# Kernel tuning notes

Measured on AMD Instinct MI355X. Metric: run time of the kernel, lower is better.

Reference implementation:

```python
import jax, jax.numpy as jnp
import numpy as np

N_BINS = 10
A_CONST = 0.4
C_CONST = 500.0


def entropy(v, n=N_BINS):
    # Faithful to the torch loop: p_i = mean(v >= lo + i*s and v < lo + (i+1)*s),
    # entropy -= p*log(p) for p != 0. Vectorized over the n bins.
    v = v.reshape(-1)
    lo = v.min()
    hi = v.max()
    scale = (hi - lo) / n
    idx = jnp.arange(n, dtype=v.dtype)
    lower = lo + idx * scale                    # [n]
    upper = lower + scale                       # [n]
    mask = (v[None, :] >= lower[:, None]) & (v[None, :] < upper[:, None])  # [n, len(v)]
    p = mask.sum(axis=1).astype(v.dtype) / v.shape[0]
    safe_p = jnp.where(p > 0, p, 1.0)
    return -jnp.sum(jnp.where(p > 0, p * jnp.log(safe_p), 0.0))


def unite(p_i, p_j, w_assess, b_assess):
    # w_local = sigmoid(Linear(|p_i - p_j|)); w_global scalar from entropy gap.
    w_local = jax.nn.sigmoid(jnp.abs(p_i - p_j) @ w_assess.T + b_assess)
    w_global = A_CONST / jnp.pi * jnp.arctan(C_CONST * (entropy(p_i) - entropy(p_j))) + 0.5
    w = w_global * w_local + (1.0 - w_global)
    return p_i * w + p_j * (1.0 - w)


def setup_inputs() -> dict:
    key = jax.random.key(0)
    ks = jax.random.split(key, 11)
    B, S, H, L = 64, 512, 1024, 3
    s = 1.0 / np.sqrt(H)
    return {
        "x": jax.random.normal(ks[0], (B, S, H), jnp.float32),
        "base_dense_w": jax.random.normal(ks[1], (H, H), jnp.float32) * s,
        "base_dense_b": jax.random.normal(ks[2], (H,), jnp.float32) * s,
        "base_out_w": jax.random.normal(ks[3], (L, H), jnp.float32) * s,
        "base_out_b": jax.random.normal(ks[4], (L,), jnp.float32) * s,
        "graft_dense_w": jax.random.normal(ks[5], (H, H), jnp.float32) * s,
        "graft_out_w": jax.random.normal(ks[6], (L, H), jnp.float32) * s,
        "dense_assess_w": jax.random.normal(ks[7], (H, H), jnp.float32) * s,
        "dense_assess_b": jax.random.normal(ks[8], (H,), jnp.float32) * s,
        "out_assess_w": jax.random.normal(ks[9], (H, H), jnp.float32) * s,
        "out_assess_b": jax.random.normal(ks[10], (H,), jnp.float32) * s,
    }


def reference(x, base_dense_w, base_dense_b, base_out_w, base_out_b,
              graft_dense_w, graft_out_w,
              dense_assess_w, dense_assess_b, out_assess_w, out_assess_b):
    # roberta branch; dropout is identity (eval mode)
    h = x[:, 0, :]  # [B, H] CLS token
    # layer 0: dense
    pu0 = unite(base_dense_w, graft_dense_w, dense_assess_w, dense_assess_b)
    h = jnp.tanh(h @ pu0.T + base_dense_b)
    # layer 1: out_proj (final -> return)
    pu1 = unite(base_out_w, graft_out_w, out_assess_w, out_assess_b)
    return h @ pu1.T + base_out_b
```

## Files before the change

kernel.cpp:

```cpp
#include <hip/hip_runtime.h>
#include <hip/hip_bf16.h>
#include <math.h>


#define NBINS 10
typedef short bf8v __attribute__((ext_vector_type(8)));
typedef float f32x4 __attribute__((ext_vector_type(4)));

#define AST(p, v) __hip_atomic_store((p), (v), __ATOMIC_RELAXED, __HIP_MEMORY_SCOPE_AGENT)
#define ALD(p)    __hip_atomic_load((p), __ATOMIC_RELAXED, __HIP_MEMORY_SCOPE_AGENT)

static __device__ __forceinline__ unsigned short f2bf(float f) {
    __hip_bfloat16 h = __float2bfloat16(f);
    return __builtin_bit_cast(unsigned short, h);
}

#define GL2LDS(gp, lp) __builtin_amdgcn_global_load_lds(                       \
    (__attribute__((address_space(1))) void*)(gp),                             \
    (__attribute__((address_space(3))) void*)(lp), 16, 0, 0)

static __device__ __forceinline__ void stage_slot(const unsigned short* __restrict__ src,
                                                  short* dst, int s, int row0, int k0) {
    int r = s >> 3, g = (s & 7) ^ (r & 7);
    GL2LDS(src + (size_t)(row0 + r) * 1024 + k0 + g * 8, dst + s * 8);
}
static __device__ __forceinline__ bf8v fr(const short* lds, int row, int G) {
    return ((const bf8v*)lds)[row * 8 + (G ^ (row & 7))];
}

static __device__ __forceinline__ float ent_bins(const unsigned* bins, float N) {
    float s = 0.0f;
    for (int b = 0; b < NBINS; b++) {
        float p = __fdiv_rn((float)ALD(&bins[b]), N);
        if (p > 0.0f) s += p * logf(p);
    }
    return -s;
}

__global__ __launch_bounds__(256) void k_prep(
    const float* __restrict__ x, const float* __restrict__ bdw, const float* __restrict__ bow,
    const float* __restrict__ gdw, const float* __restrict__ gow, const float* __restrict__ daw,
    const float* __restrict__ oaw, char* __restrict__ ws) {
    const int blk = blockIdx.x, t = threadIdx.x;
    const int lane = t & 63, wid = t >> 6;
    float* ws_f = (float*)ws;
    unsigned* ws_u = (unsigned*)ws;
    float* slots = ws_f + 576;
    float* S1    = ws_f + 1600;
    unsigned short* Db  = (unsigned short*)(ws + 4227072);
    unsigned short* Wb  = (unsigned short*)(ws + 6324224);
    unsigned short* x0b = (unsigned short*)(ws + 8421376);
    __shared__ float sp[256];
    __shared__ float s_small[16];

    if (blk < 256) {
        float lo0 = INFINITY, hi0 = -INFINITY, lo1 = INFINITY, hi1 = -INFINITY;
        int fbase = blk * 1024 + t;
#pragma unroll
        for (int q = 0; q < 4; q++) {
            int idx = fbase + q * 256;
            float4 a = ((const float4*)bdw)[idx];
            float4 b = ((const float4*)gdw)[idx];
            float4 w = ((const float4*)daw)[idx];
            lo0 = fminf(lo0, fminf(fminf(a.x, a.y), fminf(a.z, a.w)));
            hi0 = fmaxf(hi0, fmaxf(fmaxf(a.x, a.y), fmaxf(a.z, a.w)));
            lo1 = fminf(lo1, fminf(fminf(b.x, b.y), fminf(b.z, b.w)));
            hi1 = fmaxf(hi1, fmaxf(fmaxf(b.x, b.y), fmaxf(b.z, b.w)));
            ushort4 d, ww;
            d.x = f2bf(fabsf(a.x - b.x)); d.y = f2bf(fabsf(a.y - b.y));
            d.z = f2bf(fabsf(a.z - b.z)); d.w = f2bf(fabsf(a.w - b.w));
            ww.x = f2bf(w.x); ww.y = f2bf(w.y); ww.z = f2bf(w.z); ww.w = f2bf(w.w);
            ((ushort4*)Db)[idx] = d;
            ((ushort4*)Wb)[idx] = ww;
        }
        for (int off = 32; off; off >>= 1) {
            lo0 = fminf(lo0, __shfl_down(lo0, off));
            hi0 = fmaxf(hi0, __shfl_down(hi0, off));
            lo1 = fminf(lo1, __shfl_down(lo1, off));
            hi1 = fmaxf(hi1, __shfl_down(hi1, off));
        }
        if (lane == 0) { s_small[wid] = lo0; s_small[4 + wid] = hi0; s_small[8 + wid] = lo1; s_small[12 + wid] = hi1; }
        __syncthreads();
        if (t == 0) {
            slots[blk]       = fminf(fminf(s_small[0], s_small[1]), fminf(s_small[2], s_small[3]));
            slots[256 + blk] = fmaxf(fmaxf(s_small[4], s_small[5]), fmaxf(s_small[6], s_small[7]));
            slots[512 + blk] = fminf(fminf(s_small[8], s_small[9]), fminf(s_small[10], s_small[11]));
            slots[768 + blk] = fmaxf(fmaxf(s_small[12], s_small[13]), fmaxf(s_small[14], s_small[15]));
        }
    } else {
        const int blk2 = blk - 256;
        {
            int d = t >> 4, kq = t & 15;
            if (d < 12) {
                int r = d >> 2, c = blk2 * 4 + (d & 3);
                const float4* bo4 = (const float4*)(bow + r * 1024);
                const float4* go4 = (const float4*)(gow + r * 1024);
                const float4* oa4 = (const float4*)(oaw + c * 1024);
                float s = 0.f;
#pragma unroll
                for (int k4 = kq * 16; k4 < kq * 16 + 16; ++k4) {
                    float4 bv = bo4[k4], gv = go4[k4], wv = oa4[k4];
                    s += fabsf(bv.x - gv.x) * wv.x + fabsf(bv.y - gv.y) * wv.y +
                         fabsf(bv.z - gv.z) * wv.z + fabsf(bv.w - gv.w) * wv.w;
                }
                sp[t] = s;
            }
            __syncthreads();
            if (t < 12) {
                float s = 0.f;
#pragma unroll
                for (int q = 0; q < 16; q++) s += sp[t * 16 + q];
                S1[(t >> 2) * 1024 + blk2 * 4 + (t & 3)] = s;
            }
        }
        if (blk == 256 || blk == 257) {
            const float* p = (blk == 256) ? bow : gow;
            float lo = INFINITY, hi = -INFINITY;
#pragma unroll
            for (int q = 0; q < 12; q++) { float v = p[q * 256 + t]; lo = fminf(lo, v); hi = fmaxf(hi, v); }
            for (int off = 32; off; off >>= 1) { lo = fminf(lo, __shfl_down(lo, off)); hi = fmaxf(hi, __shfl_down(hi, off)); }
            __syncthreads();
            if (lane == 0) { s_small[wid] = lo; s_small[4 + wid] = hi; }
            __syncthreads();
            if (t == 0) {
                ws_f[8 + 2 * (blk - 256)] = fminf(fminf(s_small[0], s_small[1]), fminf(s_small[2], s_small[3]));
                ws_f[9 + 2 * (blk - 256)] = fmaxf(fmaxf(s_small[4], s_small[5]), fmaxf(s_small[6], s_small[7]));
            }
        }
        if (blk == 258) {
            ws_u[64 + t] = 0u;
            ws_u[320 + t] = 0u;
            if (t < 40) ws_u[16 + t] = 0u;
        }
        if (blk >= 260 && blk < 324) {
            int row = blk - 260;
            float4 v = ((const float4*)(x + (size_t)row * 524288))[t];
            ushort4 o; o.x = f2bf(v.x); o.y = f2bf(v.y); o.z = f2bf(v.z); o.w = f2bf(v.w);
            ((ushort4*)x0b)[row * 256 + t] = o;
        }
    }
}

__global__ __launch_bounds__(256) void k_main(
    const float* __restrict__ bdw, const float* __restrict__ gdw, const float* __restrict__ dab,
    const float* __restrict__ bow, const float* __restrict__ gow, const float* __restrict__ oab,
    char* __restrict__ ws) {
    const int blk = blockIdx.x, t = threadIdx.x;
    const int lane = t & 63, wid = t >> 6;
    const int lr = lane & 15, k8 = lane >> 4;
    const int wr = wid >> 1, wc = wid & 1;

    float* ws_f = (float*)ws;
    unsigned* ws_u = (unsigned*)ws;
    unsigned* bins  = ws_u + 16;
    unsigned* flags = ws_u + 64;
    float* slots = ws_f + 576;
    float* S1    = ws_f + 1600;
    float* pu1   = ws_f + 4736;
    float* part2 = ws_f + 8192;
    const unsigned short* Db  = (const unsigned short*)(ws + 4227072);
    const unsigned short* Wb  = (const unsigned short*)(ws + 6324224);
    const unsigned short* x0b = (const unsigned short*)(ws + 8421376);

    __shared__ short lds_a[2][2048];
    __shared__ short lds_b[2][4096];
    __shared__ short ldsT[32 * 72];
    __shared__ float s_small[16];
    __shared__ unsigned s_hist[NBINS];
    __shared__ float s_wg[2];

    {
        int m, b0, nb;
        if (blk < 240)      { m = 0; b0 = blk;       nb = 240; }
        else if (blk < 480) { m = 1; b0 = blk - 240; nb = 240; }
        else if (blk < 496) { m = 2; b0 = blk - 480; nb = 16; }
        else                { m = 3; b0 = blk - 496; nb = 16; }
        const float* p = (m == 0) ? bdw : (m == 1) ? gdw : (m == 2) ? bow : gow;
        int n = (m < 2) ? 1048576 : 3072;
        float lo, hi;
        if (m < 2) {
            float l = slots[m * 512 + t];
            float h = slots[m * 512 + 256 + t];
            for (int off = 32; off; off >>= 1) { l = fminf(l, __shfl_down(l, off)); h = fmaxf(h, __shfl_down(h, off)); }
            if (lane == 0) { s_small[wid] = l; s_small[4 + wid] = h; }
            __syncthreads();
            lo = fminf(fminf(s_small[0], s_small[1]), fminf(s_small[2], s_small[3]));
            hi = fmaxf(fmaxf(s_small[4], s_small[5]), fmaxf(s_small[6], s_small[7]));
        } else {
            lo = ws_f[8 + 2 * (m - 2)];
            hi = ws_f[9 + 2 * (m - 2)];
        }
        float scale = __fdiv_rn(__fsub_rn(hi, lo), 10.0f);
        float lower[NBINS], upper[NBINS];
#pragma unroll
        for (int b = 0; b < NBINS; b++) {
            lower[b] = __fadd_rn(lo, __fmul_rn((float)b, scale));
            upper[b] = __fadd_rn(lower[b], scale);
        }
        unsigned cn[NBINS] = {};
#pragma unroll 4
        for (int i = b0 * 256 + t; i < n; i += nb * 256) {
            float v = p[i];
#pragma unroll
            for (int b = 0; b < NBINS; b++)
                if (v >= lower[b] && v < upper[b]) cn[b]++;
        }
        if (t < NBINS) s_hist[t] = 0;
        __syncthreads();
#pragma unroll
        for (int b = 0; b < NBINS; b++)
            if (cn[b]) atomicAdd(&s_hist[b], cn[b]);
        __syncthreads();
        if (t < NBINS && s_hist[t])
            __hip_atomic_fetch_add(&bins[m * NBINS + t], s_hist[t], __ATOMIC_RELAXED, __HIP_MEMORY_SCOPE_AGENT);
    }
    __syncthreads();
    if (t == 0) AST(&flags[blk], 1u);

    const int c8 = blk & 7, rr = blk >> 3;
    const int bi = ((c8 >> 1) << 3) | (rr >> 3);
    const int bj = ((c8 & 1) << 3) | (rr & 7);
    f32x4 acc0 = {0.f, 0.f, 0.f, 0.f}, acc1 = {0.f, 0.f, 0.f, 0.f};
    {
        stage_slot(Db, lds_a[0], t, bi * 32, 0);
        stage_slot(Wb, lds_b[0], t, bj * 64, 0);
        stage_slot(Wb, lds_b[0], t + 256, bj * 64, 0);
        int cur = 0;
        for (int tt = 0; tt < 16; ++tt) {
            __syncthreads();
            if (tt + 1 < 16) {
                int k0 = (tt + 1) * 64;
                stage_slot(Db, lds_a[cur ^ 1], t, bi * 32, k0);
                stage_slot(Wb, lds_b[cur ^ 1], t, bj * 64, k0);
                stage_slot(Wb, lds_b[cur ^ 1], t + 256, bj * 64, k0);
            }
#pragma unroll
            for (int kk = 0; kk < 2; kk++) {
                bf8v a  = fr(lds_a[cur], wr * 16 + lr, kk * 4 + k8);
                bf8v b0 = fr(lds_b[cur], wc * 32 + lr, kk * 4 + k8);
                bf8v b1 = fr(lds_b[cur], wc * 32 + 16 + lr, kk * 4 + k8);
                acc0 = __builtin_amdgcn_mfma_f32_16x16x32_bf16(a, b0, acc0, 0, 0, 0);
                acc1 = __builtin_amdgcn_mfma_f32_16x16x32_bf16(a, b1, acc1, 0, 0, 0);
            }
            cur ^= 1;
        }
    }

    for (;;) {
        unsigned v0 = ALD(&flags[t]);
        unsigned v1 = ALD(&flags[t + 256]);
        if (__syncthreads_and((int)(v0 >= 1u && v1 >= 1u))) break;
        __builtin_amdgcn_s_sleep(1);
    }
    if (t == 0) {
        float e0 = ent_bins(&bins[0], 1048576.0f);
        float e1 = ent_bins(&bins[10], 1048576.0f);
        float e2 = ent_bins(&bins[20], 3072.0f);
        float e3 = ent_bins(&bins[30], 3072.0f);
        const float API = (float)(0.4 / M_PI);
        s_wg[0] = API * atanf(500.0f * (e0 - e1)) + 0.5f;
        s_wg[1] = API * atanf(500.0f * (e2 - e3)) + 0.5f;
    }
    __syncthreads();

    {
        float wg = s_wg[0];
#pragma unroll
        for (int j = 0; j < 2; j++) {
            f32x4 a = j ? acc1 : acc0;
#pragma unroll
            for (int r = 0; r < 4; r++) {
                int il = wr * 16 + k8 * 4 + r;
                int jl = wc * 32 + j * 16 + lr;
                int ig = bi * 32 + il, jg = bj * 64 + jl;
                float s = a[r] + dab[jg];
                float wl = 1.0f / (1.0f + expf(-s));
                float w = wg * wl + (1.0f - wg);
                float o = bdw[ig * 1024 + jg] * w + gdw[ig * 1024 + jg] * (1.0f - w);
                ldsT[il * 72 + jl] = (short)f2bf(o);
            }
        }
        __syncthreads();
        f32x4 ah0 = {0.f, 0.f, 0.f, 0.f}, ah1 = {0.f, 0.f, 0.f, 0.f};
#pragma unroll
        for (int ks = 0; ks < 2; ks++) {
            int cl = wc * 16 + lr;
            bf8v b = *(const bf8v*)&ldsT[cl * 72 + ks * 32 + k8 * 8];
            bf8v a0 = *(const bf8v*)&x0b[(wr * 32 + lr) * 1024 + bj * 64 + ks * 32 + k8 * 8];
            bf8v a1 = *(const bf8v*)&x0b[(wr * 32 + 16 + lr) * 1024 + bj * 64 + ks * 32 + k8 * 8];
            ah0 = __builtin_amdgcn_mfma_f32_16x16x32_bf16(a0, b, ah0, 0, 0, 0);
            ah1 = __builtin_amdgcn_mfma_f32_16x16x32_bf16(a1, b, ah1, 0, 0, 0);
        }
#pragma unroll
        for (int mi = 0; mi < 2; mi++) {
            f32x4 ah = mi ? ah1 : ah0;
#pragma unroll
            for (int r = 0; r < 4; r++) {
                int m = wr * 32 + mi * 16 + k8 * 4 + r;
                int cg = bi * 32 + wc * 16 + lr;
                part2[((size_t)(bj * 64 + m) << 10) + cg] = ah[r];
            }
        }
    }
    if (blk < 16 && t < 192) {
        int r = t >> 6, c = blk * 64 + (t & 63);
        float s1 = S1[r * 1024 + c];
        float wl = 1.0f / (1.0f + expf(-(s1 + oab[c])));
        float wg = s_wg[1];
        float w = wg * wl + (1.0f - wg);
        pu1[r * 1024 + c] = bow[r * 1024 + c] * w + gow[r * 1024 + c] * (1.0f - w);
    }
}

__global__ __launch_bounds__(256) void k_out(
    const float* __restrict__ bdb, const float* __restrict__ bob,
    float* __restrict__ out, const char* __restrict__ ws) {
    const int m = blockIdx.x, t = threadIdx.x;
    const int lane = t & 63, wid = t >> 6;
    const float* ws_f = (const float*)ws;
    const float* pu1   = ws_f + 4736;
    const float* part2 = ws_f + 8192;
    __shared__ float s_small[16];

    const int c0 = t * 4;
    f32x4 s = {0.f, 0.f, 0.f, 0.f};
#pragma unroll
    for (int b = 0; b < 16; b++)
        s += *(const f32x4*)(part2 + ((size_t)(b * 64 + m) << 10) + c0);
    float h0 = tanhf(s[0] + bdb[c0]);
    float h1 = tanhf(s[1] + bdb[c0 + 1]);
    float h2 = tanhf(s[2] + bdb[c0 + 2]);
    float h3 = tanhf(s[3] + bdb[c0 + 3]);
    float p0, p1, p2;
    {
        f32x4 q0 = *(const f32x4*)(pu1 + c0);
        f32x4 q1 = *(const f32x4*)(pu1 + 1024 + c0);
        f32x4 q2 = *(const f32x4*)(pu1 + 2048 + c0);
        p0 = h0 * q0[0] + h1 * q0[1] + h2 * q0[2] + h3 * q0[3];
        p1 = h0 * q1[0] + h1 * q1[1] + h2 * q1[2] + h3 * q1[3];
        p2 = h0 * q2[0] + h1 * q2[1] + h2 * q2[2] + h3 * q2[3];
    }
    for (int off = 32; off; off >>= 1) {
        p0 += __shfl_down(p0, off);
        p1 += __shfl_down(p1, off);
        p2 += __shfl_down(p2, off);
    }
    if (lane == 0) { s_small[wid] = p0; s_small[4 + wid] = p1; s_small[8 + wid] = p2; }
    __syncthreads();
    if (t == 0) {
        out[m * 3 + 0] = s_small[0] + s_small[1] + s_small[2] + s_small[3] + bob[0];
        out[m * 3 + 1] = s_small[4] + s_small[5] + s_small[6] + s_small[7] + bob[1];
        out[m * 3 + 2] = s_small[8] + s_small[9] + s_small[10] + s_small[11] + bob[2];
    }
}

extern "C" void kernel_launch(void* const* d_in, const int* in_sizes, int n_in,
                              void* d_out, int out_size, void* d_ws, size_t ws_size,
                              hipStream_t stream) {
    const float* x   = (const float*)d_in[0];
    const float* bdw = (const float*)d_in[1];
    const float* bdb = (const float*)d_in[2];
    const float* bow = (const float*)d_in[3];
    const float* bob = (const float*)d_in[4];
    const float* gdw = (const float*)d_in[5];
    const float* gow = (const float*)d_in[6];
    const float* daw = (const float*)d_in[7];
    const float* dab = (const float*)d_in[8];
    const float* oaw = (const float*)d_in[9];
    const float* oab = (const float*)d_in[10];
    float* out = (float*)d_out;
    char* ws = (char*)d_ws;

    k_prep<<<512, 256, 0, stream>>>(x, bdw, bow, gdw, gow, daw, oaw, ws);
    k_main<<<512, 256, 0, stream>>>(bdw, gdw, dab, bow, gow, oab, ws);
    k_out<<<64, 256, 0, stream>>>(bdb, bob, out, ws);
}
```

Baseline: 55.10 us.

## Fuse output kernel into main kernel via a second grid-wide flag barrier

Removes the separate k_out launch by having the first 64 blocks of k_main spin on a second set of per-block flags, then reduce the split-K partials, apply tanh and the 3-output projection in place. Partial-sum tiles are first staged through LDS and written as coalesced 64-bit atomic stores so they are visible across blocks. The workspace layout is shifted to make room for the new flags. This saves one kernel launch and its gap, at the cost of a spin wait that relies on all 512 blocks being co-resident.

```diff
diff --git a/kernel.cpp b/kernel.cpp
--- a/kernel.cpp
+++ b/kernel.cpp
@@ -6,6 +6,7 @@
 #define NBINS 10
 typedef short bf8v __attribute__((ext_vector_type(8)));
 typedef float f32x4 __attribute__((ext_vector_type(4)));
+typedef unsigned long long u64;
 
 #define AST(p, v) __hip_atomic_store((p), (v), __ATOMIC_RELAXED, __HIP_MEMORY_SCOPE_AGENT)
 #define ALD(p)    __hip_atomic_load((p), __ATOMIC_RELAXED, __HIP_MEMORY_SCOPE_AGENT)
@@ -45,11 +46,11 @@
     const int lane = t & 63, wid = t >> 6;
     float* ws_f = (float*)ws;
     unsigned* ws_u = (unsigned*)ws;
-    float* slots = ws_f + 576;
-    float* S1    = ws_f + 1600;
-    unsigned short* Db  = (unsigned short*)(ws + 4227072);
-    unsigned short* Wb  = (unsigned short*)(ws + 6324224);
-    unsigned short* x0b = (unsigned short*)(ws + 8421376);
+    float* slots = ws_f + 1088;
+    float* S1    = ws_f + 2112;
+    unsigned short* Db  = (unsigned short*)(ws + 4456448);
+    unsigned short* Wb  = (unsigned short*)(ws + 6553600);
+    unsigned short* x0b = (unsigned short*)(ws + 8650752);
     __shared__ float sp[256];
     __shared__ float s_small[16];
 
@@ -128,8 +129,8 @@
             }
         }
         if (blk == 258) {
-            ws_u[64 + t] = 0u;
-            ws_u[320 + t] = 0u;
+#pragma unroll
+            for (int q = 0; q < 4; q++) ws_u[64 + q * 256 + t] = 0u;
             if (t < 40) ws_u[16 + t] = 0u;
         }
         if (blk >= 260 && blk < 324) {
@@ -144,7 +145,8 @@
 __global__ __launch_bounds__(256) void k_main(
     const float* __restrict__ bdw, const float* __restrict__ gdw, const float* __restrict__ dab,
     const float* __restrict__ bow, const float* __restrict__ gow, const float* __restrict__ oab,
-    char* __restrict__ ws) {
+    const float* __restrict__ bdb, const float* __restrict__ bob,
+    float* __restrict__ out, char* __restrict__ ws) {
     const int blk = blockIdx.x, t = threadIdx.x;
     const int lane = t & 63, wid = t >> 6;
     const int lr = lane & 15, k8 = lane >> 4;
@@ -152,19 +154,21 @@
 
     float* ws_f = (float*)ws;
     unsigned* ws_u = (unsigned*)ws;
-    unsigned* bins  = ws_u + 16;
-    unsigned* flags = ws_u + 64;
-    float* slots = ws_f + 576;
-    float* S1    = ws_f + 1600;
-    float* pu1   = ws_f + 4736;
-    float* part2 = ws_f + 8192;
-    const unsigned short* Db  = (const unsigned short*)(ws + 4227072);
-    const unsigned short* Wb  = (const unsigned short*)(ws + 6324224);
-    const unsigned short* x0b = (const unsigned short*)(ws + 8421376);
+    unsigned* bins   = ws_u + 16;
+    unsigned* flags1 = ws_u + 64;
+    unsigned* flags2 = ws_u + 576;
+    float* slots = ws_f + 1088;
+    float* S1    = ws_f + 2112;
+    float* pu1   = ws_f + 5248;
+    float* part2 = ws_f + 16384;
+    const unsigned short* Db  = (const unsigned short*)(ws + 4456448);
+    const unsigned short* Wb  = (const unsigned short*)(ws + 6553600);
+    const unsigned short* x0b = (const unsigned short*)(ws + 8650752);
 
     __shared__ short lds_a[2][2048];
     __shared__ short lds_b[2][4096];
     __shared__ short ldsT[32 * 72];
+    __shared__ float ldsP[64 * 33];
     __shared__ float s_small[16];
     __shared__ unsigned s_hist[NBINS];
     __shared__ float s_wg[2];
@@ -215,7 +219,7 @@
             __hip_atomic_fetch_add(&bins[m * NBINS + t], s_hist[t], __ATOMIC_RELAXED, __HIP_MEMORY_SCOPE_AGENT);
     }
     __syncthreads();
-    if (t == 0) AST(&flags[blk], 1u);
+    if (t == 0) AST(&flags1[blk], 1u);
 
     const int c8 = blk & 7, rr = blk >> 3;
     const int bi = ((c8 >> 1) << 3) | (rr >> 3);
@@ -247,8 +251,8 @@
     }
 
     for (;;) {
-        unsigned v0 = ALD(&flags[t]);
-        unsigned v1 = ALD(&flags[t + 256]);
+        unsigned v0 = ALD(&flags1[t]);
+        unsigned v1 = ALD(&flags1[t + 256]);
         if (__syncthreads_and((int)(v0 >= 1u && v1 >= 1u))) break;
         __builtin_amdgcn_s_sleep(1);
     }
@@ -295,10 +299,18 @@
         for (int mi = 0; mi < 2; mi++) {
             f32x4 ah = mi ? ah1 : ah0;
 #pragma unroll
-            for (int r = 0; r < 4; r++) {
-                int m = wr * 32 + mi * 16 + k8 * 4 + r;
-                int cg = bi * 32 + wc * 16 + lr;
-                part2[((size_t)(bj * 64 + m) << 10) + cg] = ah[r];
+            for (int r = 0; r < 4; r++)
+                ldsP[(wr * 32 + mi * 16 + k8 * 4 + r) * 33 + wc * 16 + lr] = ah[r];
+        }
+        __syncthreads();
+        {
+            int m = t >> 2, c0 = (t & 3) * 8;
+            const float* row = &ldsP[m * 33 + c0];
+            float* gp = part2 + ((size_t)(bj * 64 + m) << 10) + bi * 32 + c0;
+#pragma unroll
+            for (int q = 0; q < 4; q++) {
+                u64 u = ((u64)__float_as_uint(row[2 * q + 1]) << 32) | __float_as_uint(row[2 * q]);
+                AST((u64*)(gp + 2 * q), u);
             }
         }
     }
@@ -308,49 +320,56 @@
         float wl = 1.0f / (1.0f + expf(-(s1 + oab[c])));
         float wg = s_wg[1];
         float w = wg * wl + (1.0f - wg);
-        pu1[r * 1024 + c] = bow[r * 1024 + c] * w + gow[r * 1024 + c] * (1.0f - w);
-    }
-}
-
-__global__ __launch_bounds__(256) void k_out(
-    const float* __restrict__ bdb, const float* __restrict__ bob,
-    float* __restrict__ out, const char* __restrict__ ws) {
-    const int m = blockIdx.x, t = threadIdx.x;
-    const int lane = t & 63, wid = t >> 6;
-    const float* ws_f = (const float*)ws;
-    const float* pu1   = ws_f + 4736;
-    const float* part2 = ws_f + 8192;
-    __shared__ float s_small[16];
-
-    const int c0 = t * 4;
-    f32x4 s = {0.f, 0.f, 0.f, 0.f};
-#pragma unroll
-    for (int b = 0; b < 16; b++)
-        s += *(const f32x4*)(part2 + ((size_t)(b * 64 + m) << 10) + c0);
-    float h0 = tanhf(s[0] + bdb[c0]);
-    float h1 = tanhf(s[1] + bdb[c0 + 1]);
-    float h2 = tanhf(s[2] + bdb[c0 + 2]);
-    float h3 = tanhf(s[3] + bdb[c0 + 3]);
-    float p0, p1, p2;
-    {
-        f32x4 q0 = *(const f32x4*)(pu1 + c0);
-        f32x4 q1 = *(const f32x4*)(pu1 + 1024 + c0);
-        f32x4 q2 = *(const f32x4*)(pu1 + 2048 + c0);
-        p0 = h0 * q0[0] + h1 * q0[1] + h2 * q0[2] + h3 * q0[3];
-        p1 = h0 * q1[0] + h1 * q1[1] + h2 * q1[2] + h3 * q1[3];
-        p2 = h0 * q2[0] + h1 * q2[1] + h2 * q2[2] + h3 * q2[3];
-    }
-    for (int off = 32; off; off >>= 1) {
-        p0 += __shfl_down(p0, off);
-        p1 += __shfl_down(p1, off);
-        p2 += __shfl_down(p2, off);
-    }
-    if (lane == 0) { s_small[wid] = p0; s_small[4 + wid] = p1; s_small[8 + wid] = p2; }
+        AST(&pu1[r * 1024 + c], bow[r * 1024 + c] * w + gow[r * 1024 + c] * (1.0f - w));
+    }
     __syncthreads();
-    if (t == 0) {
-        out[m * 3 + 0] = s_small[0] + s_small[1] + s_small[2] + s_small[3] + bob[0];
-        out[m * 3 + 1] = s_small[4] + s_small[5] + s_small[6] + s_small[7] + bob[1];
-        out[m * 3 + 2] = s_small[8] + s_small[9] + s_small[10] + s_small[11] + bob[2];
+    if (t == 0) AST(&flags2[blk], 1u);
+
+    if (blk < 64) {
+        for (;;) {
+            unsigned v0 = ALD(&flags2[t]);
+            unsigned v1 = ALD(&flags2[t + 256]);
+            if (__syncthreads_and((int)(v0 >= 1u && v1 >= 1u))) break;
+            __builtin_amdgcn_s_sleep(1);
+        }
+        const int m = blk, c0 = t * 4;
+        float s0 = 0, s1 = 0, s2 = 0, s3 = 0;
+#pragma unroll
+        for (int b = 0; b < 16; b++) {
+            const float* pp = part2 + ((size_t)(b * 64 + m) << 10) + c0;
+            u64 u0 = ALD((const u64*)pp);
+            u64 u1 = ALD((const u64*)(pp + 2));
+            s0 += __uint_as_float((unsigned)u0); s1 += __uint_as_float((unsigned)(u0 >> 32));
+            s2 += __uint_as_float((unsigned)u1); s3 += __uint_as_float((unsigned)(u1 >> 32));
+        }
+        float h0 = tanhf(s0 + bdb[c0]);
+        float h1 = tanhf(s1 + bdb[c0 + 1]);
+        float h2 = tanhf(s2 + bdb[c0 + 2]);
+        float h3 = tanhf(s3 + bdb[c0 + 3]);
+        float p0, p1, p2;
+        {
+            u64 a0 = ALD((const u64*)(pu1 + c0)),        a1 = ALD((const u64*)(pu1 + c0 + 2));
+            u64 b0 = ALD((const u64*)(pu1 + 1024 + c0)), b1 = ALD((const u64*)(pu1 + 1024 + c0 + 2));
+            u64 d0 = ALD((const u64*)(pu1 + 2048 + c0)), d1 = ALD((const u64*)(pu1 + 2048 + c0 + 2));
+            p0 = h0 * __uint_as_float((unsigned)a0) + h1 * __uint_as_float((unsigned)(a0 >> 32)) +
+                 h2 * __uint_as_float((unsigned)a1) + h3 * __uint_as_float((unsigned)(a1 >> 32));
+            p1 = h0 * __uint_as_float((unsigned)b0) + h1 * __uint_as_float((unsigned)(b0 >> 32)) +
+                 h2 * __uint_as_float((unsigned)b1) + h3 * __uint_as_float((unsigned)(b1 >> 32));
+            p2 = h0 * __uint_as_float((unsigned)d0) + h1 * __uint_as_float((unsigned)(d0 >> 32)) +
+                 h2 * __uint_as_float((unsigned)d1) + h3 * __uint_as_float((unsigned)(d1 >> 32));
+        }
+        for (int off = 32; off; off >>= 1) {
+            p0 += __shfl_down(p0, off);
+            p1 += __shfl_down(p1, off);
+            p2 += __shfl_down(p2, off);
+        }
+        if (lane == 0) { s_small[wid] = p0; s_small[4 + wid] = p1; s_small[8 + wid] = p2; }
+        __syncthreads();
+        if (t == 0) {
+            out[m * 3 + 0] = s_small[0] + s_small[1] + s_small[2] + s_small[3] + bob[0];
+            out[m * 3 + 1] = s_small[4] + s_small[5] + s_small[6] + s_small[7] + bob[1];
+            out[m * 3 + 2] = s_small[8] + s_small[9] + s_small[10] + s_small[11] + bob[2];
+        }
     }
 }
 
@@ -372,6 +391,5 @@
     char* ws = (char*)d_ws;
 
     k_prep<<<512, 256, 0, stream>>>(x, bdw, bow, gdw, gow, daw, oaw, ws);
-    k_main<<<512, 256, 0, stream>>>(bdw, gdw, dab, bow, gow, oab, ws);
-    k_out<<<64, 256, 0, stream>>>(bdb, bob, out, ws);
-}
+    k_main<<<512, 256, 0, stream>>>(bdw, gdw, dab, bow, gow, oab, bdb, bob, out, ws);
+}
```

Result: slower. 57.12 us (+3.7%).
